# Performance work log

Measured on AMD Instinct MI355X. Metric: run time of the kernel, lower is better.

Reference implementation:

```python
import jax, jax.numpy as jnp
import numpy as np

LAM = 0.003  # kernel_lam squash threshold


def setup_inputs() -> dict:
    key = jax.random.key(0)
    k1, k2, k3, k4 = jax.random.split(key, 4)
    B, L, H, Lk = 2, 4096, 2048, 128
    u = jax.random.normal(k1, (B, L, H), jnp.float32)
    # LongConvKernel parameter [channels=1, H, Lk]; scaled so squash keeps most taps nonzero
    kernel = jax.random.normal(k2, (1, H, Lk), jnp.float32) * 0.05
    D = jax.random.normal(k3, (1, H), jnp.float32)  # skip term [channels, H]
    # output_linear: nn.Linear(H, 2H) followed by GLU(dim=-1)
    W = jax.random.normal(k4, (2 * H, H), jnp.float32) / np.sqrt(H)
    b = jnp.zeros((2 * H,), jnp.float32)
    return {"u": u, "kernel": kernel, "D": D, "W": W, "b": b}


def reference(u, kernel, D, W, b):
    # u: [B, L, H] -> transpose to [B, H, L]
    B, L, H = u.shape
    ut = jnp.transpose(u, (0, 2, 1)).astype(jnp.float32)  # bhl
    # LongConvKernel forward: squash k = relu(|k| - lam) * sign(k)
    k = jnp.maximum(jnp.abs(kernel) - LAM, 0.0) * jnp.sign(kernel)  # [C, H, Lk]
    Lk = kernel.shape[-1]
    n = Lk + L  # FFT size for linear (causal) convolution
    k_f = jnp.fft.rfft(k, n=n)          # [C, H, n//2+1]
    u_f = jnp.fft.rfft(ut, n=n)         # [B, H, n//2+1]
    y_f = jnp.einsum('bhl,chl->bchl', u_f, k_f)
    y = jnp.fft.irfft(y_f, n=n)[..., :L]  # [B, C, H, L]
    # source adds the D skip term twice (duplicated line) -> factor 2
    y = y + 2.0 * jnp.einsum('bhl,ch->bchl', ut, D)
    # rearrange 'b c h l -> b (c h) l' then transpose -> [B, L, C*H]
    y = jnp.transpose(y.reshape(B, -1, L), (0, 2, 1))
    y = jax.nn.gelu(y, approximate=False)  # torch GELU is exact erf
    z = y @ W.T + b                     # [B, L, 2H]
    a, g = jnp.split(z, 2, axis=-1)     # GLU along last dim
    return a * jax.nn.sigmoid(g)        # [B, L, H]
```

## Files before the change

### kernel.cpp

```cpp
#include <hip/hip_runtime.h>
#include <hip/hip_bf16.h>
#include <cstdint>

constexpr int Bc  = 2;
constexpr int Lc  = 4096;
constexpr int Hc  = 2048;
constexpr int LKc = 128;
constexpr float LAMc = 0.003f;

typedef __attribute__((ext_vector_type(8))) __bf16 bf16x8;
typedef __attribute__((ext_vector_type(4))) float  f32x4;
typedef __attribute__((ext_vector_type(8))) unsigned short ushort8;

__device__ __forceinline__ unsigned short f2bf_bits(float v) {
  union { __hip_bfloat16 b; unsigned short u; } cv;
  cv.b = __float2bfloat16(v);
  return cv.u;
}
__device__ __forceinline__ float bf_bits2f(unsigned short u) {
  union { unsigned int i; float f; } cv;
  cv.i = ((unsigned int)u) << 16;
  return cv.f;
}

__device__ __forceinline__ void gl_lds16(const void* g, void* lds) {
  __builtin_amdgcn_global_load_lds(
      (const __attribute__((address_space(1))) uint32_t*)(uintptr_t)g,
      (__attribute__((address_space(3))) uint32_t*)(uint32_t)(uintptr_t)lds,
      16, 0, 0);
}

__global__ __launch_bounds__(256) void tapfrag_kernel(
    const float* __restrict__ kin, unsigned short* __restrict__ Afr) {
  const int idx  = blockIdx.x * 256 + threadIdx.x;
  const int lane = idx & 63;
  const int idx2 = idx >> 6;
  const int h  = idx2 / 5;
  const int cc = idx2 - h * 5;
  const int m = lane & 15, quad = lane >> 4;
  const int jb = m + 32 * cc - 32 + 8 * quad;
  ushort8 o;
#pragma unroll
  for (int jj = 0; jj < 8; ++jj) {
    const int j = jb + jj;
    float v = 0.f;
    if (j >= 0 && j < LKc) {
      const float x = kin[h * LKc + j];
      const float a = fabsf(x) - LAMc;
      v = (a > 0.f) ? copysignf(a, x) : 0.f;
    }
    o[jj] = f2bf_bits(v);
  }
  ((ushort8*)Afr)[idx] = o;
}

__global__ __launch_bounds__(256) void wcast_kernel(
    const float* __restrict__ W, __hip_bfloat16* __restrict__ Wb) {
  const int idx = (blockIdx.x * 256 + threadIdx.x) * 4;
  const float4 v = *(const float4*)(W + idx);
  Wb[idx + 0] = __float2bfloat16(v.x);
  Wb[idx + 1] = __float2bfloat16(v.y);
  Wb[idx + 2] = __float2bfloat16(v.z);
  Wb[idx + 3] = __float2bfloat16(v.w);
}

__global__ __launch_bounds__(256) void conv_mfma_kernel(
    const float* __restrict__ u, const unsigned short* __restrict__ Afr,
    const float* __restrict__ Dp, unsigned short* __restrict__ Am) {
  __shared__ __align__(16) unsigned short ur[16 * 664];
  __shared__ __align__(16) unsigned short ot[512 * 17];

  const int t    = threadIdx.x;
  const int lane = t & 63;
  const int wv   = t >> 6;
  const int l16  = lane & 15;
  const int quad = lane >> 4;
  const int l0 = blockIdx.x * 512;
  const int h0 = blockIdx.y * 16;
  const int b  = blockIdx.z;

  const size_t ubase = (size_t)b * Lc * Hc + h0;

#pragma unroll 4
  for (int i = 0; i < 41; ++i) {
    const int e  = (i << 8) + t;
    const int hl = e & 15;
    const int x  = e >> 4;
    const int l  = l0 + 528 - x;
    float v = 0.f;
    if (l >= 0) v = u[ubase + (size_t)min(l, Lc - 1) * Hc + hl];
    ur[hl * 664 + x] = f2bf_bits(v);
  }
  __syncthreads();

#pragma unroll 1
  for (int hi = 0; hi < 4; ++hi) {
    const int hl = (wv << 2) | hi;
    const int h  = h0 + hl;
    bf16x8 af[5];
    const unsigned short* afp = Afr + ((size_t)(h * 5) * 64 + lane) * 8;
#pragma unroll
    for (int cc = 0; cc < 5; ++cc) af[cc] = *(const bf16x8*)(afp + cc * 512);
    const float dv = 2.f * Dp[h];
    const unsigned short* urh = &ur[hl * 664];
#pragma unroll
    for (int nt = 0; nt < 2; ++nt) {
      f32x4 acc = f32x4{0.f, 0.f, 0.f, 0.f};
      const int bbase = 496 - 256 * nt - 16 * l16 + 8 * quad;
#pragma unroll
      for (int cc = 0; cc < 5; ++cc) {
        const bf16x8 bf = *(const bf16x8*)(urh + bbase + 32 * cc);
        acc = __builtin_amdgcn_mfma_f32_16x16x32_bf16(af[cc], bf, acc, 0, 0, 0);
      }
#pragma unroll
      for (int r = 0; r < 4; ++r) {
        const int lc = quad * 4 + r + 16 * l16;
        const float uu = bf_bits2f(urh[528 - 256 * nt - lc]);
        const float y = fmaf(dv, uu, acc[r]);
        const float g = 0.5f * y * (1.f + erff(y * 0.70710678118654752f));
        ot[(nt * 256 + lc) * 17 + hl] = f2bf_bits(g);
      }
    }
  }
  __syncthreads();

#pragma unroll
  for (int rr = 0; rr < 2; ++rr) {
    const int lc = (rr << 8) + t;
    const unsigned short* row = &ot[lc * 17];
    unsigned int w[8];
#pragma unroll
    for (int p = 0; p < 8; ++p)
      w[p] = (unsigned int)row[2 * p] | ((unsigned int)row[2 * p + 1] << 16);
    unsigned short* dst = Am + ((size_t)(b * Lc + l0 + lc)) * Hc + h0;
    *(uint4*)(dst)     = make_uint4(w[0], w[1], w[2], w[3]);
    *(uint4*)(dst + 8) = make_uint4(w[4], w[5], w[6], w[7]);
  }
}

constexpr int KTILES = Hc / 32;

__global__ __launch_bounds__(512, 2) void gemm_glu_kernel(
    const __hip_bfloat16* __restrict__ A, const __hip_bfloat16* __restrict__ Wb,
    const float* __restrict__ bias, float* __restrict__ out) {
  __shared__ __align__(16) char lds[131072];

  const int t    = threadIdx.x;
  const int lane = t & 63;
  const int w    = t >> 6;
  const int l16  = lane & 15;
  const int quad = lane >> 4;
  const int wr   = w >> 2;
  const int wc   = w & 3;

  const int bid = blockIdx.x;
  const int wg  = (bid & 7) * 64 + (bid >> 3);
  const int m0g = (wg & 31) * 256;
  const int n0  = (wg >> 5) * 128;

  const __hip_bfloat16* gsrc[4];
#pragma unroll
  for (int u = 0; u < 2; ++u) {
    const int f = u * 8 + w;
    gsrc[u] = A + (size_t)(m0g + f * 16 + l16) * Hc + quad * 8;
    const int wrow = ((f >> 1) & 1) * Hc + n0 + (f >> 2) * 32 + (f & 1) * 16 + l16;
    gsrc[2 + u] = Wb + (size_t)wrow * Hc + quad * 8;
  }

  f32x4 acc[8][4];
#pragma unroll
  for (int i = 0; i < 8; ++i)
#pragma unroll
    for (int j = 0; j < 4; ++j) acc[i][j] = f32x4{0.f, 0.f, 0.f, 0.f};

#define STAGE(tile, idx)                                                      \
  gl_lds16(gsrc[idx] + (size_t)(tile) * 32,                                   \
           lds + ((tile) & 3) * 32768 + (((idx) >> 1) & 1) * 16384 +          \
               (((idx) & 1) * 8 + w) * 1024)

#pragma unroll
  for (int i = 0; i < 4; ++i) STAGE(0, i);
#pragma unroll
  for (int i = 0; i < 4; ++i) STAGE(1, i);
  asm volatile("s_waitcnt vmcnt(4)" ::: "memory");
  __builtin_amdgcn_s_barrier();

  const char* sAbase = lds + wr * 8192 + lane * 16;
  const char* sBbase = lds + 16384 + wc * 4096 + lane * 16;

#define KTILE_BODY(KT, DO_STAGE, VMN)                                         \
  {                                                                           \
    const char* sA = sAbase + ((KT) & 3) * 32768;                             \
    const char* sB = sBbase + ((KT) & 3) * 32768;                             \
    bf16x8 afr[4], bfr[4];                                                    \
    _Pragma("unroll") for (int i = 0; i < 4; ++i)                             \
        afr[i] = *(const bf16x8*)(sA + i * 1024);                             \
    _Pragma("unroll") for (int i = 0; i < 4; ++i)                             \
        bfr[i] = *(const bf16x8*)(sB + i * 1024);                             \
    if (DO_STAGE) { STAGE((KT) + 2, 0); STAGE((KT) + 2, 1); }                 \
    __builtin_amdgcn_sched_barrier(0);                                        \
    __builtin_amdgcn_s_barrier();                                             \
    asm volatile("s_waitcnt lgkmcnt(0)" ::: "memory");                        \
    __builtin_amdgcn_sched_barrier(0);                                        \
    __builtin_amdgcn_s_setprio(1);                                            \
    _Pragma("unroll") for (int mf = 0; mf < 4; ++mf)                          \
        _Pragma("unroll") for (int nf = 0; nf < 4; ++nf)                      \
            acc[mf][nf] = __builtin_amdgcn_mfma_f32_16x16x32_bf16(            \
                afr[mf], bfr[nf], acc[mf][nf], 0, 0, 0);                      \
    __builtin_amdgcn_s_setprio(0);                                            \
    __builtin_amdgcn_sched_barrier(0);                                        \
    __builtin_amdgcn_s_barrier();                                             \
    _Pragma("unroll") for (int i = 0; i < 4; ++i)                             \
        afr[i] = *(const bf16x8*)(sA + (4 + i) * 1024);                       \
    if (DO_STAGE) { STAGE((KT) + 2, 2); STAGE((KT) + 2, 3); }                 \
    __builtin_amdgcn_sched_barrier(0);                                        \
    __builtin_amdgcn_s_barrier();                                             \
    asm volatile("s_waitcnt lgkmcnt(0)" ::: "memory");                        \
    __builtin_amdgcn_sched_barrier(0);                                        \
    __builtin_amdgcn_s_setprio(1);                                            \
    _Pragma("unroll") for (int mf = 0; mf < 4; ++mf)                          \
        _Pragma("unroll") for (int nf = 0; nf < 4; ++nf)                      \
            acc[4 + mf][nf] = __builtin_amdgcn_mfma_f32_16x16x32_bf16(        \
                afr[mf], bfr[nf], acc[4 + mf][nf], 0, 0, 0);                  \
    __builtin_amdgcn_s_setprio(0);                                            \
    asm volatile("s_waitcnt vmcnt(" #VMN ")" ::: "memory");                   \
    __builtin_amdgcn_sched_barrier(0);                                        \
    __builtin_amdgcn_s_barrier();                                             \
  }

#pragma unroll 1
  for (int kt = 0; kt < KTILES - 2; ++kt) KTILE_BODY(kt, true, 4)
  KTILE_BODY(KTILES - 2, false, 0)
  KTILE_BODY(KTILES - 1, false, 0)
#undef KTILE_BODY
#undef STAGE

  const int mwb = m0g + wr * 128 + quad * 4;
  const int nb  = n0 + wc * 32 + l16;
#pragma unroll
  for (int j = 0; j < 2; ++j) {
    const int n = nb + j * 16;
    const float ba = bias[n];
    const float bg = bias[Hc + n];
#pragma unroll
    for (int mf = 0; mf < 8; ++mf) {
#pragma unroll
      for (int r = 0; r < 4; ++r) {
        const float a = acc[mf][j][r] + ba;
        const float g = acc[mf][j + 2][r] + bg;
        out[(size_t)(mwb + mf * 16 + r) * Hc + n] = a * (1.f / (1.f + expf(-g)));
      }
    }
  }
}

extern "C" void kernel_launch(void* const* d_in, const int* in_sizes, int n_in,
                              void* d_out, int out_size, void* d_ws, size_t ws_size,
                              hipStream_t stream) {
  const float* u    = (const float*)d_in[0];
  const float* kin  = (const float*)d_in[1];
  const float* Dp   = (const float*)d_in[2];
  const float* W    = (const float*)d_in[3];
  const float* bias = (const float*)d_in[4];
  float* out = (float*)d_out;

  char* ws = (char*)d_ws;
  unsigned short* Afr = (unsigned short*)ws;
  __hip_bfloat16* Wb  = (__hip_bfloat16*)ws;
  unsigned short* Am  = (unsigned short*)(ws + (16 << 20));

  tapfrag_kernel<<<(Hc * 5 * 64) / 256, 256, 0, stream>>>(kin, Afr);
  conv_mfma_kernel<<<dim3(Lc / 512, Hc / 16, Bc), 256, 0, stream>>>(u, Afr, Dp, Am);
  wcast_kernel<<<(2 * Hc * Hc) / 1024, 256, 0, stream>>>(W, Wb);
  gemm_glu_kernel<<<dim3((Bc * Lc / 256) * (Hc / 128)), 512, 0, stream>>>(
      (const __hip_bfloat16*)Am, Wb, bias, out);
}
```

Baseline: 359.6 us.

## Collapse k-tile body into single barrier phase and unroll main loop by four

Each k-tile iteration used to run two half-phases, each with its own LDS fragment load, two staging calls, barriers and 16 MFMAs. Now all 8 A fragments load at once, all four staging loads are issued together, and 32 MFMAs run behind a single barrier per tile. The main loop is also manually unrolled by four so the LDS buffer offsets become constants. The aim is to cut barrier and waitcnt overhead. The cost is higher VGPR pressure from holding 8 A fragments, which may lower occupancy. The lgkmcnt wait and scheduling barriers before the MFMAs were removed, so the compiler now has to insert the LDS waits itself.

```diff
diff --git a/kernel.cpp b/kernel.cpp
--- a/kernel.cpp
+++ b/kernel.cpp
@@ -192,46 +192,37 @@
   {                                                                           \
     const char* sA = sAbase + ((KT) & 3) * 32768;                             \
     const char* sB = sBbase + ((KT) & 3) * 32768;                             \
-    bf16x8 afr[4], bfr[4];                                                    \
-    _Pragma("unroll") for (int i = 0; i < 4; ++i)                             \
-        afr[i] = *(const bf16x8*)(sA + i * 1024);                             \
+    bf16x8 afr[8], bfr[4];                                                    \
     _Pragma("unroll") for (int i = 0; i < 4; ++i)                             \
         bfr[i] = *(const bf16x8*)(sB + i * 1024);                             \
-    if (DO_STAGE) { STAGE((KT) + 2, 0); STAGE((KT) + 2, 1); }                 \
-    __builtin_amdgcn_sched_barrier(0);                                        \
-    __builtin_amdgcn_s_barrier();                                             \
-    asm volatile("s_waitcnt lgkmcnt(0)" ::: "memory");                        \
-    __builtin_amdgcn_sched_barrier(0);                                        \
+    _Pragma("unroll") for (int i = 0; i < 8; ++i)                             \
+        afr[i] = *(const bf16x8*)(sA + i * 1024);                             \
+    if (DO_STAGE) {                                                           \
+      STAGE((KT) + 2, 0); STAGE((KT) + 2, 1);                                 \
+      STAGE((KT) + 2, 2); STAGE((KT) + 2, 3);                                 \
+    }                                                                         \
     __builtin_amdgcn_s_setprio(1);                                            \
-    _Pragma("unroll") for (int mf = 0; mf < 4; ++mf)                          \
+    _Pragma("unroll") for (int mf = 0; mf < 8; ++mf)                          \
         _Pragma("unroll") for (int nf = 0; nf < 4; ++nf)                      \
             acc[mf][nf] = __builtin_amdgcn_mfma_f32_16x16x32_bf16(            \
                 afr[mf], bfr[nf], acc[mf][nf], 0, 0, 0);                      \
     __builtin_amdgcn_s_setprio(0);                                            \
-    __builtin_amdgcn_sched_barrier(0);                                        \
+    asm volatile("s_waitcnt vmcnt(" #VMN ")" ::: "memory");                   \
     __builtin_amdgcn_s_barrier();                                             \
-    _Pragma("unroll") for (int i = 0; i < 4; ++i)                             \
-        afr[i] = *(const bf16x8*)(sA + (4 + i) * 1024);                       \
-    if (DO_STAGE) { STAGE((KT) + 2, 2); STAGE((KT) + 2, 3); }                 \
-    __builtin_amdgcn_sched_barrier(0);                                        \
-    __builtin_amdgcn_s_barrier();                                             \
-    asm volatile("s_waitcnt lgkmcnt(0)" ::: "memory");                        \
-    __builtin_amdgcn_sched_barrier(0);                                        \
-    __builtin_amdgcn_s_setprio(1);                                            \
-    _Pragma("unroll") for (int mf = 0; mf < 4; ++mf)                          \
-        _Pragma("unroll") for (int nf = 0; nf < 4; ++nf)                      \
-            acc[4 + mf][nf] = __builtin_amdgcn_mfma_f32_16x16x32_bf16(        \
-                afr[mf], bfr[nf], acc[4 + mf][nf], 0, 0, 0);                  \
-    __builtin_amdgcn_s_setprio(0);                                            \
-    asm volatile("s_waitcnt vmcnt(" #VMN ")" ::: "memory");                   \
-    __builtin_amdgcn_sched_barrier(0);                                        \
-    __builtin_amdgcn_s_barrier();                                             \
   }
 
 #pragma unroll 1
-  for (int kt = 0; kt < KTILES - 2; ++kt) KTILE_BODY(kt, true, 4)
-  KTILE_BODY(KTILES - 2, false, 0)
-  KTILE_BODY(KTILES - 1, false, 0)
+  for (int k4 = 0; k4 < 15; ++k4) {
+    const int kt = k4 * 4;
+    KTILE_BODY(kt + 0, true, 4)
+    KTILE_BODY(kt + 1, true, 4)
+    KTILE_BODY(kt + 2, true, 4)
+    KTILE_BODY(kt + 3, true, 4)
+  }
+  KTILE_BODY(60, true, 4)
+  KTILE_BODY(61, true, 4)
+  KTILE_BODY(62, false, 0)
+  KTILE_BODY(63, false, 0)
 #undef KTILE_BODY
 #undef STAGE
 
```

New measurement: 359.5 us. About the same (-0.0%).
